# Kernel optimization log

Measured on AMD Instinct MI355X. Metric: run time of the kernel, lower is better.

Reference implementation:

```python
import jax, jax.numpy as jnp
import numpy as np
import math

VOCAB = 256
EMBED = 1024
HEADS = 16
MAX_SEQ = 1024
B, S = 4, 1024
EPS = 1e-5


def setup_inputs() -> dict:
    key = jax.random.key(0)
    ks = jax.random.split(key, 10)
    x = jax.random.randint(ks[0], (B, S), 0, VOCAB)
    token_embedding = jax.random.normal(ks[1], (VOCAB, EMBED), dtype=jnp.float32)
    # positional phase buffer: pos * (1/10000**(dim/E)) * pi
    pos = jnp.arange(MAX_SEQ, dtype=jnp.float32)[:, None]
    dim = jnp.arange(EMBED, dtype=jnp.float32)[None, :]
    freq = 1.0 / (10000.0 ** (dim / EMBED))
    pos_phase = pos * freq * math.pi  # [MAX_SEQ, EMBED]
    hd = EMBED // HEADS
    q_rot = jax.random.uniform(ks[2], (HEADS, hd), minval=-math.pi, maxval=math.pi)
    k_rot = jax.random.uniform(ks[3], (HEADS, hd), minval=-math.pi, maxval=math.pi)
    v_rot = jax.random.uniform(ks[4], (HEADS, hd), minval=-math.pi, maxval=math.pi)
    # orthogonal-ish init for ff_real via QR
    a = jax.random.normal(ks[5], (EMBED, EMBED), dtype=jnp.float32)
    ff_real, _ = jnp.linalg.qr(a)
    ff_imag = jax.random.uniform(ks[6], (EMBED, EMBED), minval=-0.01, maxval=0.01)
    lim = 1.0 / math.sqrt(EMBED)
    ro_real_w = jax.random.uniform(ks[7], (VOCAB, EMBED), minval=-lim, maxval=lim)
    ro_real_b = jnp.zeros((VOCAB,), dtype=jnp.float32)
    ro_imag_w = jax.random.uniform(ks[8], (VOCAB, EMBED), minval=-lim, maxval=lim)
    ro_imag_b = jnp.zeros((VOCAB,), dtype=jnp.float32)
    return {
        "x": x,
        "token_embedding": token_embedding,
        "pos_phase": pos_phase,
        "q_rot": q_rot,
        "k_rot": k_rot,
        "v_rot": v_rot,
        "ff_real": ff_real,
        "ff_imag": ff_imag,
        "ro_real_w": ro_real_w,
        "ro_real_b": ro_real_b,
        "ro_imag_w": ro_imag_w,
        "ro_imag_b": ro_imag_b,
    }


def complex_norm(z):
    mag = jnp.abs(z)
    mean_mag = jnp.mean(mag, axis=-1, keepdims=True)
    std_mag = jnp.std(mag, axis=-1, keepdims=True, ddof=1)  # torch std is unbiased
    norm_mag = (mag - mean_mag) / (std_mag + EPS)
    scale = jnp.tanh(norm_mag) / (mag + EPS)
    return z * scale.astype(jnp.complex64)


def reference(x, token_embedding, pos_phase, q_rot, k_rot, v_rot,
              ff_real, ff_imag, ro_real_w, ro_real_b, ro_imag_w, ro_imag_b):
    b, s = x.shape
    h, hd = q_rot.shape
    mag = jnp.tanh(token_embedding[x])                       # [B,S,E]
    state = mag.astype(jnp.complex64) * jnp.exp(1j * pos_phase[:s].astype(jnp.complex64))[None]
    sh = state.reshape(b, s, h, hd)                          # [B,S,H,hd]
    q = sh * jnp.exp(1j * q_rot.astype(jnp.complex64))
    k = sh * jnp.exp(1j * k_rot.astype(jnp.complex64))
    v = sh * jnp.exp(1j * v_rot.astype(jnp.complex64))
    # complex QK^H interference -> take real part as logits
    interference = jnp.einsum('bqhd,bkhd->bhqk', q, jnp.conj(k))
    attn_logits = interference.real / math.sqrt(hd)
    causal = jnp.tril(jnp.ones((s, s), dtype=bool))
    attn_logits = jnp.where(causal[None, None], attn_logits, -jnp.inf)
    attn_weights = jax.nn.softmax(attn_logits * 8.0, axis=-1)  # [B,H,S,S]
    attn_out = jnp.einsum('bhqk,bkhd->bqhd', attn_weights.astype(jnp.complex64), v)
    attn_out = attn_out.reshape(b, s, h * hd)
    state = state + attn_out
    ff = ff_real.astype(jnp.complex64) + 1j * ff_imag.astype(jnp.complex64)
    state = state @ ff
    state = complex_norm(state)
    return state.real @ ro_real_w.T + ro_real_b + state.imag @ ro_imag_w.T + ro_imag_b
```

## Files before the change

kernel.cpp:

```cpp
#include <hip/hip_runtime.h>
#include <math.h>

#define B_ 4
#define S_ 1024
#define E_ 1024
#define H_ 16
#define V_ 256

typedef _Float16 h8 __attribute__((ext_vector_type(8)));
typedef _Float16 h4 __attribute__((ext_vector_type(4)));
typedef float f4x __attribute__((ext_vector_type(4)));

__device__ __forceinline__ void gload16(const void* g, void* l) {
  __builtin_amdgcn_global_load_lds((const __attribute__((address_space(1))) void*)g,
                                   (__attribute__((address_space(3))) void*)l, 16, 0, 0);
}

#define MFMA32F16(a, b, c) __builtin_amdgcn_mfma_f32_16x16x32_f16(a, b, c, 0, 0, 0)

#if defined(__has_builtin)
#if __has_builtin(__builtin_amdgcn_mfma_f32_16x16x16f16)
#define MFMA16F16(a, b, c) __builtin_amdgcn_mfma_f32_16x16x16f16(a, b, c, 0, 0, 0)
#endif
#endif
#ifndef MFMA16F16
__device__ __forceinline__ f4x mfma16f16_asm(h4 a, h4 b, f4x c) {
  asm volatile("v_mfma_f32_16x16x16_f16 %0, %1, %2, %0" : "+v"(c) : "v"(a), "v"(b));
  return c;
}
#define MFMA16F16(a, b, c) mfma16f16_asm(a, b, c)
#endif

__global__ void rot_kernel(const float* __restrict__ qr, const float* __restrict__ kr,
                           const float* __restrict__ vr, float* __restrict__ tabs) {
  int i = blockIdx.x * blockDim.x + threadIdx.x;
  if (i >= 3 * 1024) return;
  int which = i >> 10;
  int j = i & 1023;
  const float* src = which == 0 ? qr : (which == 1 ? kr : vr);
  float s, c;
  sincosf(src[j], &s, &c);
  tabs[which * 2048 + j] = c;
  tabs[which * 2048 + 1024 + j] = s;
}

__global__ __launch_bounds__(256) void embed_qkv_kernel(
    const int* __restrict__ x, const float* __restrict__ te,
    const float* __restrict__ pp, const float* __restrict__ tabs,
    float* __restrict__ sr, float* __restrict__ si,
    unsigned short* __restrict__ Kd, unsigned short* __restrict__ Vd) {
  __shared__ unsigned short Kl2[4096];
  __shared__ unsigned short Vl2[4096];
  const int kt2 = blockIdx.x;
  const int bh = blockIdx.y;
  const int b = bh >> 4, h = bh & 15;
  const int tid = threadIdx.x;
  const float* qc = tabs + h * 64;
  const float* qs = tabs + 1024 + h * 64;
  const float* kc = tabs + 2048 + h * 64;
  const float* ks = tabs + 3072 + h * 64;
  #pragma unroll
  for (int p = 0; p < 8; ++p) {
    int id = p * 256 + tid;
    int sl = id >> 6;
    int dd = id & 63;
    int s = kt2 * 32 + sl;
    int e = h * 64 + dd;
    int tok = x[b * 1024 + s];
    float mm = tanhf(te[tok * 1024 + e]);
    float sn, cs;
    sincosf(pp[s * 1024 + e], &sn, &cs);
    float re = mm * cs, im = mm * sn;
    size_t g = ((size_t)(b * 1024 + s)) * 1024 + e;
    sr[g] = re;
    si[g] = im;
    float cq = qc[dd], sq = qs[dd], ck = kc[dd], sk = ks[dd];
    float cd = cq * ck + sq * sk;
    float sd = sq * ck - cq * sk;
    float kr = re * cd + im * sd;
    float ki = im * cd - re * sd;
    int t = sl >> 4, key = sl & 15;
    int c0 = dd, c1 = 64 + dd;
    #define KOFF(c) (t * 2048 + ((((c) >> 5) * 4 + (((c) >> 3) & 3)) * 16 + key) * 8 + ((c) & 7))
    *(_Float16*)&Kl2[KOFF(c0)] = (_Float16)kr;
    *(_Float16*)&Kl2[KOFF(c1)] = (_Float16)ki;
    #undef KOFF
    int kgk = key >> 2, jk = key & 3;
    #define VOFF(d) (t * 2048 + ((((d) >> 4) * 4 + kgk) * 16 + ((d) & 15)) * 4 + jk)
    *(_Float16*)&Vl2[VOFF(dd)] = (_Float16)re;
    *(_Float16*)&Vl2[VOFF(64 + dd)] = (_Float16)im;
    #undef VOFF
  }
  __syncthreads();
  unsigned short* kdst = Kd + ((size_t)(bh * 64 + kt2 * 2)) * 2048;
  unsigned short* vdst = Vd + ((size_t)(bh * 64 + kt2 * 2)) * 2048;
  #pragma unroll
  for (int p = 0; p < 2; ++p) {
    int c = p * 256 + tid;
    ((int4*)kdst)[c] = ((const int4*)Kl2)[c];
    ((int4*)vdst)[c] = ((const int4*)Vl2)[c];
  }
}

__global__ __launch_bounds__(256, 4) void attn_mfma_kernel(
    const float* __restrict__ sr, const float* __restrict__ si,
    const unsigned short* __restrict__ Kd, const unsigned short* __restrict__ Vd,
    const float* __restrict__ tabs,
    unsigned short* __restrict__ Af) {
  __shared__ __align__(16) unsigned short Klds[4096];
  __shared__ __align__(16) unsigned short Vlds[4096];
  const int flat = blockIdx.x;
  const int low = flat & 7, rest = flat >> 3;
  const int qt = rest >> 3;
  const int bh = ((rest & 7) << 3) | low;
  const int b = bh >> 4, h = bh & 15;
  const int tid = threadIdx.x, lane = tid & 63, wid = tid >> 6;
  const int cl = lane & 15, kg = lane >> 4;
  const int q0 = qt * 64, qw0 = q0 + wid * 16;

  h8 qf[4];
  {
    int q = qw0 + cl;
    const float* srow = sr + ((size_t)(b * 1024 + q)) * 1024 + h * 64;
    const float* irow = si + ((size_t)(b * 1024 + q)) * 1024 + h * 64;
    #pragma unroll
    for (int ksx = 0; ksx < 4; ++ksx) {
      int f0 = ksx * 32 + kg * 8;
      const float* src = (f0 < 64) ? (srow + f0) : (irow + (f0 - 64));
      float4 v0 = *(const float4*)src;
      float4 v1 = *(const float4*)(src + 4);
      qf[ksx][0] = (_Float16)v0.x; qf[ksx][1] = (_Float16)v0.y;
      qf[ksx][2] = (_Float16)v0.z; qf[ksx][3] = (_Float16)v0.w;
      qf[ksx][4] = (_Float16)v1.x; qf[ksx][5] = (_Float16)v1.y;
      qf[ksx][6] = (_Float16)v1.z; qf[ksx][7] = (_Float16)v1.w;
    }
  }

  f4x acc[8] = {};
  float m_ = -1e30f, l_ = 0.f;
  const int ktmax = qt * 4 + 4;
  const int wqmax = qw0 + 15;

  for (int kp = 0; kp < ktmax; kp += 2) {
    __syncthreads();
    const unsigned short* kbase = Kd + ((size_t)(bh * 64 + kp)) * 2048;
    const unsigned short* vbase = Vd + ((size_t)(bh * 64 + kp)) * 2048;
    #pragma unroll
    for (int r = 0; r < 2; ++r) {
      int c = r * 256 + wid * 64 + lane;
      gload16(kbase + (size_t)c * 8, Klds + (r * 256 + wid * 64) * 8);
      gload16(vbase + (size_t)c * 8, Vlds + (r * 256 + wid * 64) * 8);
    }
    __syncthreads();
    #pragma unroll
    for (int t2 = 0; t2 < 2; ++t2) {
      const int k0 = (kp + t2) * 16;
      if (k0 > wqmax) continue;
      f4x sc = {};
      #pragma unroll
      for (int ksx = 0; ksx < 4; ++ksx) {
        h8 ka = *(const h8*)&Klds[t2 * 2048 + ksx * 512 + lane * 8];
        sc = MFMA32F16(ka, qf[ksx], sc);
      }
      const int qcol = qw0 + cl;
      if (k0 + 15 > qw0) {
        #pragma unroll
        for (int r = 0; r < 4; ++r)
          if (k0 + kg * 4 + r > qcol) sc[r] = -1e30f;
      }
      float mx = fmaxf(fmaxf(sc[0], sc[1]), fmaxf(sc[2], sc[3]));
      mx = fmaxf(mx, __shfl_xor(mx, 16, 64));
      mx = fmaxf(mx, __shfl_xor(mx, 32, 64));
      float mn = fmaxf(m_, mx);
      float corr = __expf(m_ - mn);
      float p0 = __expf(sc[0] - mn), p1 = __expf(sc[1] - mn);
      float p2 = __expf(sc[2] - mn), p3 = __expf(sc[3] - mn);
      float s0 = p0 + p1 + p2 + p3;
      s0 += __shfl_xor(s0, 16, 64);
      s0 += __shfl_xor(s0, 32, 64);
      l_ = l_ * corr + s0;
      bool resc = mn > m_;
      m_ = mn;
      if (__any(resc)) {
        #pragma unroll
        for (int mt = 0; mt < 8; ++mt) acc[mt] *= corr;
      }
      h4 pb;
      pb[0] = (_Float16)p0; pb[1] = (_Float16)p1;
      pb[2] = (_Float16)p2; pb[3] = (_Float16)p3;
      #pragma unroll
      for (int mt = 0; mt < 8; ++mt) {
        h4 va = *(const h4*)&Vlds[t2 * 2048 + mt * 256 + lane * 4];
        acc[mt] = MFMA16F16(va, pb, acc[mt]);
      }
    }
  }
  {
    float linv = 1.0f / l_;
    int q = qw0 + cl;
    size_t mrow = (size_t)(b * 1024 + q);
    size_t obase = mrow * 1024 + h * 64;
    size_t abase = mrow * 2048 + h * 64;
    #pragma unroll
    for (int mt = 0; mt < 4; ++mt) {
      int d0 = mt * 16 + kg * 4;
      float4 s_r = *(const float4*)&sr[obase + d0];
      float4 s_i = *(const float4*)&si[obase + d0];
      float srv[4] = {s_r.x, s_r.y, s_r.z, s_r.w};
      float siv[4] = {s_i.x, s_i.y, s_i.z, s_i.w};
      h4 hr, hi;
      #pragma unroll
      for (int r = 0; r < 4; ++r) {
        int d = d0 + r;
        float orv = acc[mt][r] * linv;
        float oiv = acc[mt + 4][r] * linv;
        float c = tabs[4096 + h * 64 + d], s = tabs[5120 + h * 64 + d];
        hr[r] = (_Float16)(orv * c - oiv * s + srv[r]);
        hi[r] = (_Float16)(orv * s + oiv * c + siv[r]);
      }
      *(h4*)&Af[abase + d0]        = hr;
      *(h4*)&Af[abase + 1024 + d0] = hi;
    }
  }
}

__global__ void split_b_kernel(const float* __restrict__ fr, const float* __restrict__ fi,
                               unsigned short* __restrict__ Bt) {
  __shared__ float tile[32][33];
  const int k0 = blockIdx.x * 32, n0 = blockIdx.y * 32;
  const int tid = threadIdx.x;
  #pragma unroll
  for (int p = 0; p < 4; ++p) {
    int e = p * 256 + tid;
    int kk = e >> 5, nn = e & 31;
    int k = k0 + kk, n = n0 + nn;
    float v;
    if (n < 1024) v = (k < 1024) ? fr[(size_t)k * 1024 + n] : -fi[(size_t)(k - 1024) * 1024 + n];
    else          v = (k < 1024) ? fi[(size_t)k * 1024 + (n - 1024)]
                                 : fr[(size_t)(k - 1024) * 1024 + (n - 1024)];
    tile[kk][nn] = v;
  }
  __syncthreads();
  #pragma unroll
  for (int p = 0; p < 4; ++p) {
    int e = p * 256 + tid;
    int nn = e >> 5, kk = e & 31;
    *(_Float16*)&Bt[(size_t)(n0 + nn) * 2048 + (k0 + kk)] = (_Float16)tile[kk][nn];
  }
}

__global__ void split_w_kernel(const float* __restrict__ wr, const float* __restrict__ wi,
                               unsigned short* __restrict__ Wt) {
  int idx = blockIdx.x * 256 + threadIdx.x;
  int v = idx >> 9;
  int k4 = (idx & 511) * 4;
  float4 a = (k4 < 1024) ? *(const float4*)&wr[(size_t)v * 1024 + k4]
                         : *(const float4*)&wi[(size_t)v * 1024 + k4 - 1024];
  h4 h;
  h[0] = (_Float16)a.x; h[1] = (_Float16)a.y;
  h[2] = (_Float16)a.z; h[3] = (_Float16)a.w;
  *(h4*)&Wt[(size_t)v * 2048 + k4] = h;
}

__global__ __launch_bounds__(256, 4) void gemm_ff(
    const unsigned short* __restrict__ A,
    const unsigned short* __restrict__ Bt,
    float* __restrict__ pr0, float* __restrict__ pi0,
    float* __restrict__ pr1, float* __restrict__ pi1) {
  __shared__ short As[128 * 64];
  __shared__ short Bs[128 * 64];
  const int tid = threadIdx.x;
  const int lane = tid & 63, wid = tid >> 6;
  const int m0 = blockIdx.x * 128, n0 = blockIdx.y * 128;
  const int z = blockIdx.z;
  const int wr = wid >> 1, wc = wid & 1;
  const int cl = lane & 15, rg = lane >> 4;

  f4x acc[4][4] = {};
  const int cbase = wid * 256;

  for (int kt = z * 16; kt < z * 16 + 16; ++kt) {
    const int k0 = kt * 64;
    #pragma unroll
    for (int it = 0; it < 4; ++it) {
      int c = cbase + it * 64 + lane;
      gload16(A + (size_t)(m0 + (c >> 3)) * 2048 + k0 + (c & 7) * 8,
              As + (cbase + it * 64) * 8);
      gload16(Bt + (size_t)(n0 + (c >> 3)) * 2048 + k0 + (c & 7) * 8,
              Bs + (cbase + it * 64) * 8);
    }
    __syncthreads();
    #pragma unroll
    for (int ks = 0; ks < 2; ++ks) {
      h8 a[4], b[4];
      #pragma unroll
      for (int ms = 0; ms < 4; ++ms)
        a[ms] = *(const h8*)&As[(wr * 64 + ms * 16 + cl) * 64 + ks * 32 + rg * 8];
      #pragma unroll
      for (int ns = 0; ns < 4; ++ns)
        b[ns] = *(const h8*)&Bs[(wc * 64 + ns * 16 + cl) * 64 + ks * 32 + rg * 8];
      #pragma unroll
      for (int ms = 0; ms < 4; ++ms)
        #pragma unroll
        for (int ns = 0; ns < 4; ++ns)
          acc[ms][ns] = MFMA32F16(a[ms], b[ns], acc[ms][ns]);
    }
    __syncthreads();
  }

  const int colbase = n0 + wc * 64;
  float* o_r = z ? pr1 : pr0;
  float* o_i = z ? pi1 : pi0;
  float* dst = (colbase < 1024) ? o_r : o_i;
  const int cb = colbase & 1023;
  #pragma unroll
  for (int ms = 0; ms < 4; ++ms)
    #pragma unroll
    for (int r2 = 0; r2 < 4; ++r2) {
      const int grow = m0 + wr * 64 + ms * 16 + rg * 4 + r2;
      #pragma unroll
      for (int ns = 0; ns < 4; ++ns)
        dst[(size_t)grow * 1024 + cb + ns * 16 + cl] = acc[ms][ns][r2];
    }
}

__global__ __launch_bounds__(256, 4) void gemm_ro(
    const unsigned short* __restrict__ Z,
    const unsigned short* __restrict__ Wt,
    float* __restrict__ part) {
  __shared__ short As[128 * 64];
  __shared__ short Bs[128 * 64];
  const int tid = threadIdx.x;
  const int lane = tid & 63, wid = tid >> 6;
  const int m0 = blockIdx.x * 128, n0 = blockIdx.y * 128;
  const int z = blockIdx.z;
  const int wr = wid >> 1, wc = wid & 1;
  const int cl = lane & 15, rg = lane >> 4;

  f4x acc[4][4] = {};
  const int cbase = wid * 256;

  for (int kt = z * 4; kt < z * 4 + 4; ++kt) {
    const int k0 = kt * 64;
    #pragma unroll
    for (int it = 0; it < 4; ++it) {
      int c = cbase + it * 64 + lane;
      gload16(Z + (size_t)(m0 + (c >> 3)) * 2048 + k0 + (c & 7) * 8,
              As + (cbase + it * 64) * 8);
      gload16(Wt + (size_t)(n0 + (c >> 3)) * 2048 + k0 + (c & 7) * 8,
              Bs + (cbase + it * 64) * 8);
    }
    __syncthreads();
    #pragma unroll
    for (int ks = 0; ks < 2; ++ks) {
      h8 a[4], b[4];
      #pragma unroll
      for (int ms = 0; ms < 4; ++ms)
        a[ms] = *(const h8*)&As[(wr * 64 + ms * 16 + cl) * 64 + ks * 32 + rg * 8];
      #pragma unroll
      for (int ns = 0; ns < 4; ++ns)
        b[ns] = *(const h8*)&Bs[(wc * 64 + ns * 16 + cl) * 64 + ks * 32 + rg * 8];
      #pragma unroll
      for (int ms = 0; ms < 4; ++ms)
        #pragma unroll
        for (int ns = 0; ns < 4; ++ns)
          acc[ms][ns] = MFMA32F16(a[ms], b[ns], acc[ms][ns]);
    }
    __syncthreads();
  }

  float* dst = part + (size_t)z * 4096 * 256;
  const int colbase = n0 + wc * 64;
  #pragma unroll
  for (int ms = 0; ms < 4; ++ms)
    #pragma unroll
    for (int r2 = 0; r2 < 4; ++r2) {
      const int grow = m0 + wr * 64 + ms * 16 + rg * 4 + r2;
      #pragma unroll
      for (int ns = 0; ns < 4; ++ns)
        dst[(size_t)grow * 256 + colbase + ns * 16 + cl] = acc[ms][ns][r2];
    }
}

__global__ __launch_bounds__(256) void norm_split_kernel(
    const float* __restrict__ pr0, const float* __restrict__ pi0,
    const float* __restrict__ pr1, const float* __restrict__ pi1,
    unsigned short* __restrict__ Z) {
  const int row = blockIdx.x, tid = threadIdx.x;
  const int base = row * E_ + tid * 4;
  float4 r0 = *(const float4*)&pr0[base];
  float4 r1 = *(const float4*)&pr1[base];
  float4 i0 = *(const float4*)&pi0[base];
  float4 i1 = *(const float4*)&pi1[base];
  float4 zr = make_float4(r0.x + r1.x, r0.y + r1.y, r0.z + r1.z, r0.w + r1.w);
  float4 zi = make_float4(i0.x + i1.x, i0.y + i1.y, i0.z + i1.z, i0.w + i1.w);
  float mg[4];
  mg[0] = sqrtf(zr.x * zr.x + zi.x * zi.x);
  mg[1] = sqrtf(zr.y * zr.y + zi.y * zi.y);
  mg[2] = sqrtf(zr.z * zr.z + zi.z * zi.z);
  mg[3] = sqrtf(zr.w * zr.w + zi.w * zi.w);
  float s1 = mg[0] + mg[1] + mg[2] + mg[3];
  float s2 = mg[0]*mg[0] + mg[1]*mg[1] + mg[2]*mg[2] + mg[3]*mg[3];
  #pragma unroll
  for (int off = 1; off < 64; off <<= 1) {
    s1 += __shfl_xor(s1, off, 64);
    s2 += __shfl_xor(s2, off, 64);
  }
  __shared__ float ws1[4], ws2[4];
  if ((tid & 63) == 0) { ws1[tid >> 6] = s1; ws2[tid >> 6] = s2; }
  __syncthreads();
  s1 = ws1[0] + ws1[1] + ws1[2] + ws1[3];
  s2 = ws2[0] + ws2[1] + ws2[2] + ws2[3];
  float mean = s1 * (1.0f / 1024.0f);
  float var = (s2 - 1024.0f * mean * mean) * (1.0f / 1023.0f);
  var = fmaxf(var, 0.0f);
  float inv_sd = 1.0f / (sqrtf(var) + 1e-5f);
  float sc[4];
  #pragma unroll
  for (int t = 0; t < 4; ++t)
    sc[t] = tanhf((mg[t] - mean) * inv_sd) / (mg[t] + 1e-5f);
  h4 hr, hi;
  hr[0] = (_Float16)(zr.x * sc[0]); hr[1] = (_Float16)(zr.y * sc[1]);
  hr[2] = (_Float16)(zr.z * sc[2]); hr[3] = (_Float16)(zr.w * sc[3]);
  hi[0] = (_Float16)(zi.x * sc[0]); hi[1] = (_Float16)(zi.y * sc[1]);
  hi[2] = (_Float16)(zi.z * sc[2]); hi[3] = (_Float16)(zi.w * sc[3]);
  const size_t zb = (size_t)row * 2048 + tid * 4;
  *(h4*)&Z[zb]        = hr;
  *(h4*)&Z[zb + 1024] = hi;
}

__global__ void reduce_bias_kernel(const float* __restrict__ part,
                                   const float* __restrict__ rb,
                                   const float* __restrict__ ib,
                                   float* __restrict__ out) {
  int i4 = (blockIdx.x * 256 + threadIdx.x) * 4;
  int col = i4 & 255;
  float4 s = *(const float4*)&part[i4];
  #pragma unroll
  for (int z = 1; z < 8; ++z) {
    float4 v = *(const float4*)&part[(size_t)z * 1048576 + i4];
    s.x += v.x; s.y += v.y; s.z += v.z; s.w += v.w;
  }
  s.x += rb[col + 0] + ib[col + 0];
  s.y += rb[col + 1] + ib[col + 1];
  s.z += rb[col + 2] + ib[col + 2];
  s.w += rb[col + 3] + ib[col + 3];
  *(float4*)&out[i4] = s;
}

extern "C" void kernel_launch(void* const* d_in, const int* in_sizes, int n_in,
                              void* d_out, int out_size, void* d_ws, size_t ws_size,
                              hipStream_t stream) {
  const int*   x    = (const int*)d_in[0];
  const float* te   = (const float*)d_in[1];
  const float* pp   = (const float*)d_in[2];
  const float* qr   = (const float*)d_in[3];
  const float* kr   = (const float*)d_in[4];
  const float* vr   = (const float*)d_in[5];
  const float* ffr  = (const float*)d_in[6];
  const float* ffi  = (const float*)d_in[7];
  const float* rorw = (const float*)d_in[8];
  const float* rorb = (const float*)d_in[9];
  const float* roiw = (const float*)d_in[10];
  const float* roib = (const float*)d_in[11];
  float* out = (float*)d_out;

  char* W = (char*)d_ws;
  const size_t MiB = 1 << 20;
  float* sr  = (float*)W;
  float* si  = (float*)(W + 16 * MiB);
  unsigned short* Af = (unsigned short*)(W + 32 * MiB);
  unsigned short* Kd = (unsigned short*)(W + 48 * MiB);
  unsigned short* Vd = (unsigned short*)(W + 64 * MiB);
  unsigned short* Bt = (unsigned short*)(W + 48 * MiB);
  unsigned short* Wt = (unsigned short*)(W + 56 * MiB);
  float* tabs = (float*)(W + 96 * MiB);
  float* pr0 = sr;
  float* pi0 = si;
  float* pr1 = (float*)(W + 64 * MiB);
  float* pi1 = (float*)(W + 80 * MiB);
  unsigned short* Zhl = Af;
  float* ro_part = (float*)(W + 64 * MiB);

  rot_kernel<<<12, 256, 0, stream>>>(qr, kr, vr, tabs);
  embed_qkv_kernel<<<dim3(32, 64), 256, 0, stream>>>(x, te, pp, tabs, sr, si, Kd, Vd);
  attn_mfma_kernel<<<1024, 256, 0, stream>>>(sr, si, Kd, Vd, tabs, Af);
  split_b_kernel<<<dim3(64, 64), 256, 0, stream>>>(ffr, ffi, Bt);
  split_w_kernel<<<512, 256, 0, stream>>>(rorw, roiw, Wt);
  gemm_ff<<<dim3(32, 16, 2), 256, 0, stream>>>(Af, Bt, pr0, pi0, pr1, pi1);
  norm_split_kernel<<<B_ * S_, 256, 0, stream>>>(pr0, pi0, pr1, pi1, Zhl);
  gemm_ro<<<dim3(32, 2, 8), 256, 0, stream>>>(Zhl, Wt, ro_part);
  reduce_bias_kernel<<<1024, 256, 0, stream>>>(ro_part, rorb, roib, out);
}
```

Measured before the change: 167.8 us.

## Double-buffer K/V tiles via register prefetch and use lazy softmax rescaling

Replaces the synchronous global-to-LDS load per key pair with a two-stage LDS double buffer. The next tile is prefetched into registers while the current one is computed, and there is a single barrier per iteration. The two 16-key subtiles are processed together with one shared max, the accumulator is rescaled only when the running max grows by more than a threshold, and MFMA sections get raised wave priority. This aims to hide global-load latency and cut barriers and rescale work, at the cost of more registers and double the LDS, which may reduce occupancy.

Result: slower. 212.6 us (+26.7%).

```diff
diff --git a/kernel.cpp b/kernel.cpp
--- a/kernel.cpp
+++ b/kernel.cpp
@@ -107,8 +107,8 @@
     const unsigned short* __restrict__ Kd, const unsigned short* __restrict__ Vd,
     const float* __restrict__ tabs,
     unsigned short* __restrict__ Af) {
-  __shared__ __align__(16) unsigned short Klds[4096];
-  __shared__ __align__(16) unsigned short Vlds[4096];
+  __shared__ __align__(16) unsigned short Klds[2][4096];
+  __shared__ __align__(16) unsigned short Vlds[2][4096];
   const int flat = blockIdx.x;
   const int low = flat & 7, rest = flat >> 3;
   const int qt = rest >> 3;
@@ -138,61 +138,111 @@
 
   f4x acc[8] = {};
   float m_ = -1e30f, l_ = 0.f;
-  const int ktmax = qt * 4 + 4;
+  const int np = qt * 2 + 2;
   const int wqmax = qw0 + 15;
-
-  for (int kp = 0; kp < ktmax; kp += 2) {
-    __syncthreads();
-    const unsigned short* kbase = Kd + ((size_t)(bh * 64 + kp)) * 2048;
-    const unsigned short* vbase = Vd + ((size_t)(bh * 64 + kp)) * 2048;
-    #pragma unroll
-    for (int r = 0; r < 2; ++r) {
-      int c = r * 256 + wid * 64 + lane;
-      gload16(kbase + (size_t)c * 8, Klds + (r * 256 + wid * 64) * 8);
-      gload16(vbase + (size_t)c * 8, Vlds + (r * 256 + wid * 64) * 8);
-    }
-    __syncthreads();
-    #pragma unroll
-    for (int t2 = 0; t2 < 2; ++t2) {
-      const int k0 = (kp + t2) * 16;
-      if (k0 > wqmax) continue;
-      f4x sc = {};
+  const int qcol = qw0 + cl;
+
+  const int4* kgbase = (const int4*)(Kd + ((size_t)(bh * 64)) * 2048);
+  const int4* vgbase = (const int4*)(Vd + ((size_t)(bh * 64)) * 2048);
+  int4 kreg[2], vreg[2];
+
+  #pragma unroll
+  for (int j = 0; j < 2; ++j) {
+    kreg[j] = kgbase[tid + 256 * j];
+    vreg[j] = vgbase[tid + 256 * j];
+  }
+  #pragma unroll
+  for (int j = 0; j < 2; ++j) {
+    ((int4*)Klds[0])[tid + 256 * j] = kreg[j];
+    ((int4*)Vlds[0])[tid + 256 * j] = vreg[j];
+  }
+  if (np > 1) {
+    #pragma unroll
+    for (int j = 0; j < 2; ++j) {
+      kreg[j] = kgbase[512 + tid + 256 * j];
+      vreg[j] = vgbase[512 + tid + 256 * j];
+    }
+  }
+  asm volatile("s_waitcnt lgkmcnt(0)" ::: "memory");
+  __builtin_amdgcn_s_barrier();
+
+  for (int p = 0; p < np; ++p) {
+    const int cur = p & 1;
+    const int k0a = p * 32;
+    if (k0a <= wqmax) {
+      __builtin_amdgcn_s_setprio(1);
+      f4x sca = {}, scb = {};
       #pragma unroll
       for (int ksx = 0; ksx < 4; ++ksx) {
-        h8 ka = *(const h8*)&Klds[t2 * 2048 + ksx * 512 + lane * 8];
-        sc = MFMA32F16(ka, qf[ksx], sc);
-      }
-      const int qcol = qw0 + cl;
-      if (k0 + 15 > qw0) {
+        h8 ka = *(const h8*)&Klds[cur][ksx * 512 + lane * 8];
+        sca = MFMA32F16(ka, qf[ksx], sca);
+      }
+      #pragma unroll
+      for (int ksx = 0; ksx < 4; ++ksx) {
+        h8 kb = *(const h8*)&Klds[cur][2048 + ksx * 512 + lane * 8];
+        scb = MFMA32F16(kb, qf[ksx], scb);
+      }
+      __builtin_amdgcn_s_setprio(0);
+      if (k0a + 31 > qw0) {
         #pragma unroll
-        for (int r = 0; r < 4; ++r)
-          if (k0 + kg * 4 + r > qcol) sc[r] = -1e30f;
-      }
-      float mx = fmaxf(fmaxf(sc[0], sc[1]), fmaxf(sc[2], sc[3]));
+        for (int r = 0; r < 4; ++r) {
+          if (k0a + kg * 4 + r > qcol)      sca[r] = -1e30f;
+          if (k0a + 16 + kg * 4 + r > qcol) scb[r] = -1e30f;
+        }
+      }
+      float mx = fmaxf(fmaxf(fmaxf(sca[0], sca[1]), fmaxf(sca[2], sca[3])),
+                       fmaxf(fmaxf(scb[0], scb[1]), fmaxf(scb[2], scb[3])));
       mx = fmaxf(mx, __shfl_xor(mx, 16, 64));
       mx = fmaxf(mx, __shfl_xor(mx, 32, 64));
-      float mn = fmaxf(m_, mx);
-      float corr = __expf(m_ - mn);
-      float p0 = __expf(sc[0] - mn), p1 = __expf(sc[1] - mn);
-      float p2 = __expf(sc[2] - mn), p3 = __expf(sc[3] - mn);
-      float s0 = p0 + p1 + p2 + p3;
+      if (!__all(mx <= m_ + 8.0f)) {
+        float mn = fmaxf(m_, mx);
+        float corr = __expf(m_ - mn);
+        #pragma unroll
+        for (int mt = 0; mt < 8; ++mt) acc[mt] *= corr;
+        l_ *= corr;
+        m_ = mn;
+      }
+      float pa0 = __expf(sca[0] - m_), pa1 = __expf(sca[1] - m_);
+      float pa2 = __expf(sca[2] - m_), pa3 = __expf(sca[3] - m_);
+      float pb0 = __expf(scb[0] - m_), pb1 = __expf(scb[1] - m_);
+      float pb2 = __expf(scb[2] - m_), pb3 = __expf(scb[3] - m_);
+      float s0 = ((pa0 + pa1) + (pa2 + pa3)) + ((pb0 + pb1) + (pb2 + pb3));
       s0 += __shfl_xor(s0, 16, 64);
       s0 += __shfl_xor(s0, 32, 64);
-      l_ = l_ * corr + s0;
-      bool resc = mn > m_;
-      m_ = mn;
-      if (__any(resc)) {
+      l_ += s0;
+      h4 pba, pbb;
+      pba[0] = (_Float16)pa0; pba[1] = (_Float16)pa1;
+      pba[2] = (_Float16)pa2; pba[3] = (_Float16)pa3;
+      pbb[0] = (_Float16)pb0; pbb[1] = (_Float16)pb1;
+      pbb[2] = (_Float16)pb2; pbb[3] = (_Float16)pb3;
+      __builtin_amdgcn_s_setprio(1);
+      #pragma unroll
+      for (int mt = 0; mt < 8; ++mt) {
+        h4 va = *(const h4*)&Vlds[cur][mt * 256 + lane * 4];
+        acc[mt] = MFMA16F16(va, pba, acc[mt]);
+      }
+      #pragma unroll
+      for (int mt = 0; mt < 8; ++mt) {
+        h4 vb = *(const h4*)&Vlds[cur][2048 + mt * 256 + lane * 4];
+        acc[mt] = MFMA16F16(vb, pbb, acc[mt]);
+      }
+      __builtin_amdgcn_s_setprio(0);
+    }
+    if (p + 1 < np) {
+      #pragma unroll
+      for (int j = 0; j < 2; ++j) {
+        ((int4*)Klds[cur ^ 1])[tid + 256 * j] = kreg[j];
+        ((int4*)Vlds[cur ^ 1])[tid + 256 * j] = vreg[j];
+      }
+      if (p + 2 < np) {
         #pragma unroll
-        for (int mt = 0; mt < 8; ++mt) acc[mt] *= corr;
-      }
-      h4 pb;
-      pb[0] = (_Float16)p0; pb[1] = (_Float16)p1;
-      pb[2] = (_Float16)p2; pb[3] = (_Float16)p3;
-      #pragma unroll
-      for (int mt = 0; mt < 8; ++mt) {
-        h4 va = *(const h4*)&Vlds[t2 * 2048 + mt * 256 + lane * 4];
-        acc[mt] = MFMA16F16(va, pb, acc[mt]);
-      }
+        for (int j = 0; j < 2; ++j) {
+          kreg[j] = kgbase[(size_t)(p + 2) * 512 + tid + 256 * j];
+          vreg[j] = vgbase[(size_t)(p + 2) * 512 + tid + 256 * j];
+        }
+      }
+      asm volatile("s_waitcnt lgkmcnt(0)" ::: "memory");
+      __builtin_amdgcn_s_barrier();
     }
   }
   {
```
